# Optimization experiments

Measured on AMD Instinct MI355X. Metric: run time of the kernel, lower is better.

Reference implementation:

```python
import jax, jax.numpy as jnp
import numpy as np

D_MODEL = 4096
D_FF = 4 * D_MODEL
B, S = 2, 2048


def setup_inputs() -> dict:
    key = jax.random.key(0)
    kx, k1, kb1, k2, kb2 = jax.random.split(key, 5)
    s1 = 1.0 / np.sqrt(D_MODEL)
    s2 = 1.0 / np.sqrt(D_FF)
    return {
        "x": jax.random.normal(kx, (B, S, D_MODEL), dtype=jnp.float32),
        "W1": jax.random.normal(k1, (D_MODEL, D_FF), dtype=jnp.float32) * s1,
        "b1": jax.random.normal(kb1, (D_FF,), dtype=jnp.float32) * 0.01,
        "W2": jax.random.normal(k2, (D_FF, D_MODEL), dtype=jnp.float32) * s2,
        "b2": jax.random.normal(kb2, (D_MODEL,), dtype=jnp.float32) * 0.01,
    }


def reference(x, W1, b1, W2, b2):
    # FlashFFN: engine computes fc2(act(fc1(x) + b1)); host then nan-guards
    # and adds fc2_bias. GELU is the standard transformer FFN activation.
    orig_shape = x.shape
    flat_x = x.reshape(-1, D_MODEL)                      # [T, D]
    h = jax.nn.gelu(flat_x @ W1 + b1)                    # [T, 4D]
    y = h @ W2                                           # [T, D]
    y = jnp.nan_to_num(y, nan=0.0, posinf=0.0, neginf=0.0)
    return y.reshape(orig_shape) + b2
```

## Files before the change

### kernel.cpp

```cpp
#include <hip/hip_runtime.h>
#include <hip/hip_bf16.h>


using bf16 = __hip_bfloat16;
typedef __attribute__((ext_vector_type(4))) float floatx4;
typedef __attribute__((ext_vector_type(8))) short shortx8;

#define TOKENS 4096
#define DMODEL 4096
#define DFF    16384

__device__ __forceinline__ void gload_lds16(const void* g, void* l) {
  __builtin_amdgcn_global_load_lds(
      (const __attribute__((address_space(1))) unsigned int*)g,
      (__attribute__((address_space(3))) unsigned int*)l,
      16, 0, 0);
}

__device__ __forceinline__ unsigned lds_u32(const void* p) {
  return (unsigned)(unsigned long long)(const __attribute__((address_space(3))) char*)p;
}

__device__ __forceinline__ float gelu_tanh(float x) {
  float z = 0.7978845608028654f * (x + 0.044715f * x * x * x);
  float e = __expf(2.0f * z);
  float t = 1.0f - 2.0f / (e + 1.0f);
  return 0.5f * x * (1.0f + t);
}

#define DSR(dst, addr, off) \
  asm volatile("ds_read_b128 %0, %1 offset:" #off : "=v"(dst) : "v"(addr))

__global__ void cvt_f32_bf16(const float* __restrict__ in, bf16* __restrict__ out) {
  int i = (blockIdx.x * blockDim.x + threadIdx.x) * 8;
  float4 a = *(const float4*)(in + i);
  float4 b = *(const float4*)(in + i + 4);
  union { shortx8 v; bf16 h[8]; } r;
  r.h[0] = __float2bfloat16(a.x); r.h[1] = __float2bfloat16(a.y);
  r.h[2] = __float2bfloat16(a.z); r.h[3] = __float2bfloat16(a.w);
  r.h[4] = __float2bfloat16(b.x); r.h[5] = __float2bfloat16(b.y);
  r.h[6] = __float2bfloat16(b.z); r.h[7] = __float2bfloat16(b.w);
  *(shortx8*)(out + i) = r.v;
}

__global__ void transpose_cvt(const float* __restrict__ in, bf16* __restrict__ out,
                              int R, int C) {
  __shared__ float tile[64][65];
  const int c0 = blockIdx.x * 64, r0 = blockIdx.y * 64;
  const int t = threadIdx.x;
#pragma unroll
  for (int p = 0; p < 4; ++p) {
    int r = p * 16 + (t >> 4);
    int c = (t & 15) * 4;
    float4 v = *(const float4*)(in + (size_t)(r0 + r) * C + c0 + c);
    tile[r][c] = v.x; tile[r][c + 1] = v.y;
    tile[r][c + 2] = v.z; tile[r][c + 3] = v.w;
  }
  __syncthreads();
#pragma unroll
  for (int p = 0; p < 2; ++p) {
    int c = p * 32 + (t >> 3);
    int rb = (t & 7) * 8;
    union { shortx8 v; bf16 h[8]; } u;
#pragma unroll
    for (int j = 0; j < 8; ++j) u.h[j] = __float2bfloat16(tile[rb + j][c]);
    *(shortx8*)(out + (size_t)(c0 + c) * R + r0 + rb) = u.v;
  }
}

template <int FUSE_GELU>
__launch_bounds__(512, 2)
__global__ void gemm_bt(const bf16* __restrict__ A, const bf16* __restrict__ Bt,
                        const float* __restrict__ bias, void* __restrict__ Cout,
                        int M, int N, int K) {
  __shared__ __align__(16) bf16 As[2 * 2 * 128 * 64];
  __shared__ __align__(16) bf16 Bs[2 * 2 * 128 * 64];

  const int tid = threadIdx.x;
  const int wave = tid >> 6;
  const int lane = tid & 63;

  const int wg8  = blockIdx.x & 255;
  const int xcd  = wg8 & 7;
  const int slot = wg8 >> 3;
  const int m0 = (2 * xcd + (slot & 1)) * 256;
  const int n0 = ((blockIdx.x >> 8) * 16 + (slot >> 1)) * 256;

  const size_t Ks = (size_t)K;
  const int NT = K >> 6;

  const int swz = (lane & 7) ^ ((lane >> 3) & 7);
  const bf16* agp = A  + (size_t)(m0 + wave * 8 + (lane >> 3)) * Ks + swz * 8;
  const bf16* bgp = Bt + (size_t)(n0 + wave * 8 + (lane >> 3)) * Ks + swz * 8;

  const int wr = wave >> 2, wc = wave & 3;
  const int fr = lane & 15;
  const int q  = lane >> 4;
  const unsigned As0 = lds_u32(As);
  const unsigned Bs0 = lds_u32(Bs);
  const unsigned aK0 = As0 + (unsigned)((wr * 16 + fr) * 128 +
                       (((fr >> 2) & 1) * 64) + ((q ^ (fr & 3)) * 16));
  const unsigned aK1 = aK0 ^ 64u;
  const unsigned bK0 = Bs0 + (unsigned)((wc * 16 + fr) * 128 +
                       (((fr >> 2) & 1) * 64) + ((q ^ (fr & 3)) * 16));
  const unsigned bK1 = bK0 ^ 64u;

  floatx4 acc[8][4] = {};

  {
    bf16* lA = As + wave * 512;
    bf16* lB = Bs + wave * 512;
    gload_lds16(agp,             lA);
    gload_lds16(agp +  64 * Ks,  lA + 4096);
    gload_lds16(bgp,             lB);
    gload_lds16(bgp +  64 * Ks,  lB + 4096);
    gload_lds16(agp + 128 * Ks,  lA + 8192);
    gload_lds16(agp + 192 * Ks,  lA + 12288);
    gload_lds16(bgp + 128 * Ks,  lB + 8192);
    gload_lds16(bgp + 192 * Ks,  lB + 12288);
  }
  asm volatile("s_waitcnt vmcnt(4)");
  __builtin_amdgcn_s_barrier();

  for (int t = 0; t < NT; ++t) {
    const unsigned dsel = (unsigned)(t & 1) << 15;
    const unsigned a0 = aK0 + dsel, a1 = aK1 + dsel;
    const unsigned b0 = bK0 + dsel, b1 = bK1 + dsel;
    const bool st = (t + 1 < NT);
    const bf16* gA = agp + (size_t)(t + 1) * 64;
    const bf16* gB = bgp + (size_t)(t + 1) * 64;
    bf16* lA = As + ((t + 1) & 1) * 16384 + wave * 512;
    bf16* lB = Bs + ((t + 1) & 1) * 16384 + wave * 512;

    shortx8 A0[2][4], A1[2][4], B0[2][2], B1[2][2];

    DSR(A0[0][0], a0, 0);     DSR(A0[0][1], a0, 4096);
    DSR(A0[0][2], a0, 8192);  DSR(A0[0][3], a0, 12288);
    DSR(A0[1][0], a1, 0);     DSR(A0[1][1], a1, 4096);
    DSR(A0[1][2], a1, 8192);  DSR(A0[1][3], a1, 12288);
    DSR(B0[0][0], b0, 0);     DSR(B0[0][1], b0, 8192);
    DSR(B0[1][0], b1, 0);     DSR(B0[1][1], b1, 8192);
    if (st) { gload_lds16(gA, lA); gload_lds16(gA + 64 * Ks, lA + 4096); }
    __builtin_amdgcn_s_barrier();
    asm volatile("s_waitcnt lgkmcnt(0)");
    __builtin_amdgcn_sched_barrier(0);
    __builtin_amdgcn_s_setprio(1);
#pragma unroll
    for (int f = 0; f < 4; ++f)
#pragma unroll
      for (int n = 0; n < 2; ++n) {
        acc[f][n] = __builtin_amdgcn_mfma_f32_16x16x32_bf16(A0[0][f], B0[0][n], acc[f][n], 0, 0, 0);
        acc[f][n] = __builtin_amdgcn_mfma_f32_16x16x32_bf16(A0[1][f], B0[1][n], acc[f][n], 0, 0, 0);
      }
    __builtin_amdgcn_s_setprio(0);
    __builtin_amdgcn_sched_barrier(0);
    if (st) asm volatile("s_waitcnt vmcnt(4)");
    else    asm volatile("s_waitcnt vmcnt(2)");
    __builtin_amdgcn_s_barrier();

    DSR(A1[0][0], a0, 16384); DSR(A1[0][1], a0, 20480);
    DSR(A1[0][2], a0, 24576); DSR(A1[0][3], a0, 28672);
    DSR(A1[1][0], a1, 16384); DSR(A1[1][1], a1, 20480);
    DSR(A1[1][2], a1, 24576); DSR(A1[1][3], a1, 28672);
    if (st) { gload_lds16(gB, lB); gload_lds16(gB + 64 * Ks, lB + 4096); }
    __builtin_amdgcn_s_barrier();
    asm volatile("s_waitcnt lgkmcnt(0)");
    __builtin_amdgcn_sched_barrier(0);
    __builtin_amdgcn_s_setprio(1);
#pragma unroll
    for (int f = 0; f < 4; ++f)
#pragma unroll
      for (int n = 0; n < 2; ++n) {
        acc[4 + f][n] = __builtin_amdgcn_mfma_f32_16x16x32_bf16(A1[0][f], B0[0][n], acc[4 + f][n], 0, 0, 0);
        acc[4 + f][n] = __builtin_amdgcn_mfma_f32_16x16x32_bf16(A1[1][f], B0[1][n], acc[4 + f][n], 0, 0, 0);
      }
    __builtin_amdgcn_s_setprio(0);
    __builtin_amdgcn_sched_barrier(0);
    if (st) asm volatile("s_waitcnt vmcnt(4)");
    else    asm volatile("s_waitcnt vmcnt(0)");
    __builtin_amdgcn_s_barrier();

    DSR(B1[0][0], b0, 16384); DSR(B1[0][1], b0, 24576);
    DSR(B1[1][0], b1, 16384); DSR(B1[1][1], b1, 24576);
    if (st) { gload_lds16(gA + 128 * Ks, lA + 8192); gload_lds16(gA + 192 * Ks, lA + 12288); }
    __builtin_amdgcn_s_barrier();
    asm volatile("s_waitcnt lgkmcnt(0)");
    __builtin_amdgcn_sched_barrier(0);
    __builtin_amdgcn_s_setprio(1);
#pragma unroll
    for (int f = 0; f < 4; ++f)
#pragma unroll
      for (int n = 0; n < 2; ++n) {
        acc[f][2 + n] = __builtin_amdgcn_mfma_f32_16x16x32_bf16(A0[0][f], B1[0][n], acc[f][2 + n], 0, 0, 0);
        acc[f][2 + n] = __builtin_amdgcn_mfma_f32_16x16x32_bf16(A0[1][f], B1[1][n], acc[f][2 + n], 0, 0, 0);
      }
    __builtin_amdgcn_s_setprio(0);
    __builtin_amdgcn_sched_barrier(0);
    __builtin_amdgcn_s_barrier();

    if (st) { gload_lds16(gB + 128 * Ks, lB + 8192); gload_lds16(gB + 192 * Ks, lB + 12288); }
    __builtin_amdgcn_s_setprio(1);
#pragma unroll
    for (int f = 0; f < 4; ++f)
#pragma unroll
      for (int n = 0; n < 2; ++n) {
        acc[4 + f][2 + n] = __builtin_amdgcn_mfma_f32_16x16x32_bf16(A1[0][f], B1[0][n], acc[4 + f][2 + n], 0, 0, 0);
        acc[4 + f][2 + n] = __builtin_amdgcn_mfma_f32_16x16x32_bf16(A1[1][f], B1[1][n], acc[4 + f][2 + n], 0, 0, 0);
      }
    __builtin_amdgcn_s_setprio(0);
    __builtin_amdgcn_sched_barrier(0);
    if (st) asm volatile("s_waitcnt vmcnt(4)");
    __builtin_amdgcn_s_barrier();
  }

  const int col0 = n0 + wc * 16 + fr;
  const int row0 = m0 + wr * 16 + (lane >> 4) * 4;
#pragma unroll
  for (int ni = 0; ni < 4; ++ni) {
    const int col = col0 + ni * 64;
    const float bv = bias[col];
#pragma unroll
    for (int mi = 0; mi < 8; ++mi) {
#pragma unroll
      for (int r = 0; r < 4; ++r) {
        const int row = row0 + mi * 32 + r;
        float v = acc[mi][ni][r];
        if (FUSE_GELU) {
          v = gelu_tanh(v + bv);
          ((bf16*)Cout)[(size_t)row * N + col] = __float2bfloat16(v);
        } else {
          if (!isfinite(v)) v = 0.0f;
          ((float*)Cout)[(size_t)row * N + col] = v + bv;
        }
      }
    }
  }
}

extern "C" void kernel_launch(void* const* d_in, const int* in_sizes, int n_in,
                              void* d_out, int out_size, void* d_ws, size_t ws_size,
                              hipStream_t stream) {
  const float* x  = (const float*)d_in[0];
  const float* W1 = (const float*)d_in[1];
  const float* b1 = (const float*)d_in[2];
  const float* W2 = (const float*)d_in[3];
  const float* b2 = (const float*)d_in[4];
  float* out = (float*)d_out;

  char* ws = (char*)d_ws;
  bf16* xb  = (bf16*)(ws);
  bf16* h   = (bf16*)(ws + (size_t)32  * 1024 * 1024);
  bf16* w1t = (bf16*)(ws + (size_t)160 * 1024 * 1024);
  bf16* w2t = (bf16*)(ws + (size_t)288 * 1024 * 1024);

  cvt_f32_bf16<<<(TOKENS * DMODEL / 8) / 256, 256, 0, stream>>>(x, xb);
  transpose_cvt<<<dim3(DFF / 64, DMODEL / 64), 256, 0, stream>>>(W1, w1t, DMODEL, DFF);
  transpose_cvt<<<dim3(DMODEL / 64, DFF / 64), 256, 0, stream>>>(W2, w2t, DFF, DMODEL);

  gemm_bt<1><<<dim3((DFF / 256) * (TOKENS / 256)), 512, 0, stream>>>(
      xb, w1t, b1, h, TOKENS, DFF, DMODEL);

  gemm_bt<0><<<dim3((DMODEL / 256) * (TOKENS / 256)), 512, 0, stream>>>(
      h, w2t, b2, out, TOKENS, DMODEL, DFF);
}
```

Measured before the change: 1.103 ms.

## Software-pipeline LDS fragment reads to overlap with MFMA quadrants

Restructures the main GEMM loop so that LDS reads of the A0/B0 fragments for the next k-tile are issued during the current tile's later MFMA quadrants. Partial lgkmcnt waits replace full ones, and several barriers are dropped, so LDS latency is hidden behind matrix math rather than stalling it. It also reorders the global-to-LDS loads and changes the vmcnt thresholds. The cost is more live registers and trickier wait-count correctness: a miscounted vmcnt or lgkmcnt could read stale LDS data.

```diff
diff --git a/kernel.cpp b/kernel.cpp
--- a/kernel.cpp
+++ b/kernel.cpp
@@ -106,6 +106,7 @@
   const unsigned bK1 = bK0 ^ 64u;
 
   floatx4 acc[8][4] = {};
+  shortx8 A0[2][4], A1[2][4], B0[2][2], B1[2][2];
 
   {
     bf16* lA = As + wave * 512;
@@ -116,55 +117,60 @@
     gload_lds16(bgp +  64 * Ks,  lB + 4096);
     gload_lds16(agp + 128 * Ks,  lA + 8192);
     gload_lds16(agp + 192 * Ks,  lA + 12288);
+    gload_lds16(bgp,             lB);
+  }
+  {
+    bf16* lB = Bs + wave * 512;
     gload_lds16(bgp + 128 * Ks,  lB + 8192);
     gload_lds16(bgp + 192 * Ks,  lB + 12288);
   }
-  asm volatile("s_waitcnt vmcnt(4)");
+  asm volatile("s_waitcnt vmcnt(3)");
   __builtin_amdgcn_s_barrier();
+  DSR(B0[0][0], bK0, 0); DSR(B0[0][1], bK0, 8192);
+  DSR(B0[1][0], bK1, 0); DSR(B0[1][1], bK1, 8192);
+  DSR(A0[0][0], aK0, 0);     DSR(A0[0][1], aK0, 4096);
+  DSR(A0[0][2], aK0, 8192);  DSR(A0[0][3], aK0, 12288);
+  DSR(A0[1][0], aK1, 0);     DSR(A0[1][1], aK1, 4096);
+  DSR(A0[1][2], aK1, 8192);  DSR(A0[1][3], aK1, 12288);
 
   for (int t = 0; t < NT; ++t) {
-    const unsigned dsel = (unsigned)(t & 1) << 15;
-    const unsigned a0 = aK0 + dsel, a1 = aK1 + dsel;
-    const unsigned b0 = bK0 + dsel, b1 = bK1 + dsel;
+    const unsigned dsel  = (unsigned)(t & 1) << 15;
+    const unsigned dseln = (unsigned)((t + 1) & 1) << 15;
+    const unsigned a0 = aK0 + dsel,  a1 = aK1 + dsel;
+    const unsigned b0 = bK0 + dsel,  b1 = bK1 + dsel;
+    const unsigned an0 = aK0 + dseln, an1 = aK1 + dseln;
+    const unsigned bn0 = bK0 + dseln, bn1 = bK1 + dseln;
     const bool st = (t + 1 < NT);
     const bf16* gA = agp + (size_t)(t + 1) * 64;
     const bf16* gB = bgp + (size_t)(t + 1) * 64;
     bf16* lA = As + ((t + 1) & 1) * 16384 + wave * 512;
     bf16* lB = Bs + ((t + 1) & 1) * 16384 + wave * 512;
 
-    shortx8 A0[2][4], A1[2][4], B0[2][2], B1[2][2];
-
-    DSR(A0[0][0], a0, 0);     DSR(A0[0][1], a0, 4096);
-    DSR(A0[0][2], a0, 8192);  DSR(A0[0][3], a0, 12288);
-    DSR(A0[1][0], a1, 0);     DSR(A0[1][1], a1, 4096);
-    DSR(A0[1][2], a1, 8192);  DSR(A0[1][3], a1, 12288);
-    DSR(B0[0][0], b0, 0);     DSR(B0[0][1], b0, 8192);
-    DSR(B0[1][0], b1, 0);     DSR(B0[1][1], b1, 8192);
-    if (st) { gload_lds16(gA, lA); gload_lds16(gA + 64 * Ks, lA + 4096); }
-    __builtin_amdgcn_s_barrier();
-    asm volatile("s_waitcnt lgkmcnt(0)");
-    __builtin_amdgcn_sched_barrier(0);
-    __builtin_amdgcn_s_setprio(1);
-#pragma unroll
-    for (int f = 0; f < 4; ++f)
-#pragma unroll
-      for (int n = 0; n < 2; ++n) {
-        acc[f][n] = __builtin_amdgcn_mfma_f32_16x16x32_bf16(A0[0][f], B0[0][n], acc[f][n], 0, 0, 0);
-        acc[f][n] = __builtin_amdgcn_mfma_f32_16x16x32_bf16(A0[1][f], B0[1][n], acc[f][n], 0, 0, 0);
-      }
-    __builtin_amdgcn_s_setprio(0);
-    __builtin_amdgcn_sched_barrier(0);
-    if (st) asm volatile("s_waitcnt vmcnt(4)");
-    else    asm volatile("s_waitcnt vmcnt(2)");
-    __builtin_amdgcn_s_barrier();
-
     DSR(A1[0][0], a0, 16384); DSR(A1[0][1], a0, 20480);
     DSR(A1[0][2], a0, 24576); DSR(A1[0][3], a0, 28672);
     DSR(A1[1][0], a1, 16384); DSR(A1[1][1], a1, 20480);
     DSR(A1[1][2], a1, 24576); DSR(A1[1][3], a1, 28672);
     if (st) { gload_lds16(gB, lB); gload_lds16(gB + 64 * Ks, lB + 4096); }
-    __builtin_amdgcn_s_barrier();
-    asm volatile("s_waitcnt lgkmcnt(0)");
+    asm volatile("s_waitcnt lgkmcnt(8)");
+    __builtin_amdgcn_sched_barrier(0);
+    __builtin_amdgcn_s_setprio(1);
+#pragma unroll
+    for (int f = 0; f < 4; ++f)
+#pragma unroll
+      for (int n = 0; n < 2; ++n) {
+        acc[f][n] = __builtin_amdgcn_mfma_f32_16x16x32_bf16(A0[0][f], B0[0][n], acc[f][n], 0, 0, 0);
+        acc[f][n] = __builtin_amdgcn_mfma_f32_16x16x32_bf16(A0[1][f], B0[1][n], acc[f][n], 0, 0, 0);
+      }
+    __builtin_amdgcn_s_setprio(0);
+    __builtin_amdgcn_sched_barrier(0);
+    if (st) asm volatile("s_waitcnt vmcnt(2)");
+    else    asm volatile("s_waitcnt vmcnt(0)");
+    __builtin_amdgcn_s_barrier();
+
+    DSR(B1[0][0], b0, 16384); DSR(B1[0][1], b0, 24576);
+    DSR(B1[1][0], b1, 16384); DSR(B1[1][1], b1, 24576);
+    if (st) { gload_lds16(gA, lA); gload_lds16(gA + 64 * Ks, lA + 4096); }
+    asm volatile("s_waitcnt lgkmcnt(4)");
     __builtin_amdgcn_sched_barrier(0);
     __builtin_amdgcn_s_setprio(1);
 #pragma unroll
@@ -176,16 +182,33 @@
       }
     __builtin_amdgcn_s_setprio(0);
     __builtin_amdgcn_sched_barrier(0);
-    if (st) asm volatile("s_waitcnt vmcnt(4)");
-    else    asm volatile("s_waitcnt vmcnt(0)");
-    __builtin_amdgcn_s_barrier();
-
-    DSR(B1[0][0], b0, 16384); DSR(B1[0][1], b0, 24576);
-    DSR(B1[1][0], b1, 16384); DSR(B1[1][1], b1, 24576);
-    if (st) { gload_lds16(gA + 128 * Ks, lA + 8192); gload_lds16(gA + 192 * Ks, lA + 12288); }
-    __builtin_amdgcn_s_barrier();
-    asm volatile("s_waitcnt lgkmcnt(0)");
-    __builtin_amdgcn_sched_barrier(0);
+    if (st) asm volatile("s_waitcnt vmcnt(2)");
+    __builtin_amdgcn_s_barrier();
+
+    if (st) {
+      DSR(B0[0][0], bn0, 0); DSR(B0[0][1], bn0, 8192);
+      DSR(B0[1][0], bn1, 0); DSR(B0[1][1], bn1, 8192);
+      gload_lds16(gA + 128 * Ks, lA + 8192);
+      gload_lds16(gA + 192 * Ks, lA + 12288);
+      asm volatile("s_waitcnt lgkmcnt(4)");
+    } else {
+      asm volatile("s_waitcnt lgkmcnt(0)");
+    }
+    __builtin_amdgcn_sched_barrier(0);
+    __builtin_amdgcn_s_setprio(1);
+#pragma unroll
+    for (int f = 0; f < 4; ++f)
+#pragma unroll
+      for (int n = 0; n < 2; ++n) {
+        acc[4 + f][2 + n] = __builtin_amdgcn_mfma_f32_16x16x32_bf16(A1[0][f], B1[0][n], acc[4 + f][2 + n], 0, 0, 0);
+        acc[4 + f][2 + n] = __builtin_amdgcn_mfma_f32_16x16x32_bf16(A1[1][f], B1[1][n], acc[4 + f][2 + n], 0, 0, 0);
+      }
+    __builtin_amdgcn_s_setprio(0);
+    __builtin_amdgcn_sched_barrier(0);
+    if (st) asm volatile("s_waitcnt vmcnt(2)");
+    __builtin_amdgcn_s_barrier();
+
+    if (st) { gload_lds16(gB + 128 * Ks, lB + 8192); gload_lds16(gB + 192 * Ks, lB + 12288); }
     __builtin_amdgcn_s_setprio(1);
 #pragma unroll
     for (int f = 0; f < 4; ++f)
@@ -196,20 +219,13 @@
       }
     __builtin_amdgcn_s_setprio(0);
     __builtin_amdgcn_sched_barrier(0);
-    __builtin_amdgcn_s_barrier();
-
-    if (st) { gload_lds16(gB + 128 * Ks, lB + 8192); gload_lds16(gB + 192 * Ks, lB + 12288); }
-    __builtin_amdgcn_s_setprio(1);
-#pragma unroll
-    for (int f = 0; f < 4; ++f)
-#pragma unroll
-      for (int n = 0; n < 2; ++n) {
-        acc[4 + f][2 + n] = __builtin_amdgcn_mfma_f32_16x16x32_bf16(A1[0][f], B1[0][n], acc[4 + f][2 + n], 0, 0, 0);
-        acc[4 + f][2 + n] = __builtin_amdgcn_mfma_f32_16x16x32_bf16(A1[1][f], B1[1][n], acc[4 + f][2 + n], 0, 0, 0);
-      }
-    __builtin_amdgcn_s_setprio(0);
-    __builtin_amdgcn_sched_barrier(0);
-    if (st) asm volatile("s_waitcnt vmcnt(4)");
+    if (st) {
+      DSR(A0[0][0], an0, 0);     DSR(A0[0][1], an0, 4096);
+      DSR(A0[0][2], an0, 8192);  DSR(A0[0][3], an0, 12288);
+      DSR(A0[1][0], an1, 0);     DSR(A0[1][1], an1, 4096);
+      DSR(A0[1][2], an1, 8192);  DSR(A0[1][3], an1, 12288);
+      asm volatile("s_waitcnt vmcnt(2)");
+    }
     __builtin_amdgcn_s_barrier();
   }
 
```

New measurement: 1.097 ms. Within noise of the previous version (-0.5%).

## Software-pipeline LDS fragment reads across K-tiles and unroll by two

Applied to the files above, without the earlier changes.

Restructures the GEMM main loop so LDS fragment reads for the next K-tile are issued during the current tile's MFMA phases, with partial lgkmcnt waits instead of full drains. Barriers per tile drop from seven to four, and B loads for tile t+2 are prefetched early. The loop is unrolled by two with compile-time LDS offsets so buffer selection needs no runtime add. This adds register pressure from fragments live across iterations and assumes NT is even. The waitcnt and barrier ordering is delicate and could race if a count is off.

```diff
diff --git a/kernel.cpp b/kernel.cpp
--- a/kernel.cpp
+++ b/kernel.cpp
@@ -28,8 +28,8 @@
   return 0.5f * x * (1.0f + t);
 }
 
-#define DSR(dst, addr, off) \
-  asm volatile("ds_read_b128 %0, %1 offset:" #off : "=v"(dst) : "v"(addr))
+#define DSRI(dst, addr, off) \
+  asm volatile("ds_read_b128 %0, %1 offset:%c2" : "=v"(dst) : "v"(addr), "i"(off))
 
 __global__ void cvt_f32_bf16(const float* __restrict__ in, bf16* __restrict__ out) {
   int i = (blockIdx.x * blockDim.x + threadIdx.x) * 8;
@@ -67,6 +67,114 @@
     *(shortx8*)(out + (size_t)(c0 + c) * R + r0 + rb) = u.v;
   }
 }
+
+#define TILE_BODY(T, D, DN)                                                     \
+  {                                                                             \
+    const int t_ = (T);                                                         \
+    const bool st  = (t_ + 1 < NT);                                             \
+    const bool st2 = (t_ + 2 < NT);                                             \
+    const bf16* gA = agp + (size_t)(t_ + 1) * 64;                               \
+    bf16* lA = As + (DN / 2) + wave * 512;                                      \
+    bf16* lB = Bs + (DN / 2) + wave * 512;                                      \
+              \
+    DSRI(A1[0][0], aK0, (D) + 16384); DSRI(A1[0][1], aK0, (D) + 20480);         \
+    DSRI(A1[0][2], aK0, (D) + 24576); DSRI(A1[0][3], aK0, (D) + 28672);         \
+    DSRI(A1[1][0], aK1, (D) + 16384); DSRI(A1[1][1], aK1, (D) + 20480);         \
+    DSRI(A1[1][2], aK1, (D) + 24576); DSRI(A1[1][3], aK1, (D) + 28672);         \
+    if (st) { gload_lds16(gA, lA); gload_lds16(gA + 64 * Ks, lA + 4096); }      \
+    asm volatile("s_waitcnt lgkmcnt(8)");      \
+    __builtin_amdgcn_sched_barrier(0);                      \
+    __builtin_amdgcn_s_setprio(1);                                              \
+    _Pragma("unroll")                                                           \
+    for (int f = 0; f < 4; ++f)                                                 \
+      _Pragma("unroll")                                                         \
+      for (int n = 0; n < 2; ++n)                                               \
+        acc[f][n] = __builtin_amdgcn_mfma_f32_16x16x32_bf16(A0[0][f], B0[0][n], acc[f][n], 0, 0, 0); \
+    _Pragma("unroll")                                                           \
+    for (int f = 0; f < 4; ++f)                                                 \
+      _Pragma("unroll")                                                         \
+      for (int n = 0; n < 2; ++n)                                               \
+        acc[f][n] = __builtin_amdgcn_mfma_f32_16x16x32_bf16(A0[1][f], B0[1][n], acc[f][n], 0, 0, 0); \
+    __builtin_amdgcn_s_setprio(0);                                              \
+    if (st) asm volatile("s_waitcnt vmcnt(4)");            \
+    else    asm volatile("s_waitcnt vmcnt(0)");                                 \
+    __builtin_amdgcn_s_barrier();                                               \
+              \
+    DSRI(B1[0][0], bK0, (D) + 16384); DSRI(B1[0][1], bK0, (D) + 24576);         \
+    DSRI(B1[1][0], bK1, (D) + 16384); DSRI(B1[1][1], bK1, (D) + 24576);         \
+    if (st) { gload_lds16(gA + 128 * Ks, lA + 8192);                            \
+              gload_lds16(gA + 192 * Ks, lA + 12288); }                         \
+    asm volatile("s_waitcnt lgkmcnt(4)");            \
+    __builtin_amdgcn_sched_barrier(0);                                          \
+    __builtin_amdgcn_s_setprio(1);                                              \
+    _Pragma("unroll")                                                           \
+    for (int f = 0; f < 4; ++f)                                                 \
+      _Pragma("unroll")                                                         \
+      for (int n = 0; n < 2; ++n)                                               \
+        acc[4 + f][n] = __builtin_amdgcn_mfma_f32_16x16x32_bf16(A1[0][f], B0[0][n], acc[4 + f][n], 0, 0, 0); \
+    _Pragma("unroll")                                                           \
+    for (int f = 0; f < 4; ++f)                                                 \
+      _Pragma("unroll")                                                         \
+      for (int n = 0; n < 2; ++n)                                               \
+        acc[4 + f][n] = __builtin_amdgcn_mfma_f32_16x16x32_bf16(A1[1][f], B0[1][n], acc[4 + f][n], 0, 0, 0); \
+    __builtin_amdgcn_s_setprio(0);                                              \
+    if (st) asm volatile("s_waitcnt vmcnt(4)");          \
+    __builtin_amdgcn_s_barrier();                                               \
+            \
+    if (st) {                                                                   \
+      const bf16* gB = bgp + (size_t)(t_ + 1) * 64;                             \
+      DSRI(B0[0][0], bK0, (DN) + 0); DSRI(B0[0][1], bK0, (DN) + 8192);          \
+      DSRI(B0[1][0], bK1, (DN) + 0); DSRI(B0[1][1], bK1, (DN) + 8192);          \
+      gload_lds16(gB + 128 * Ks, lB + 8192);                                    \
+      gload_lds16(gB + 192 * Ks, lB + 12288);                                   \
+      asm volatile("s_waitcnt lgkmcnt(4)");         \
+    } else {                                                                    \
+      asm volatile("s_waitcnt lgkmcnt(0)");                                     \
+    }                                                                           \
+    __builtin_amdgcn_sched_barrier(0);                                          \
+    __builtin_amdgcn_s_setprio(1);                                              \
+    _Pragma("unroll")                                                           \
+    for (int f = 0; f < 4; ++f)                                                 \
+      _Pragma("unroll")                                                         \
+      for (int n = 0; n < 2; ++n)                                               \
+        acc[4 + f][2 + n] = __builtin_amdgcn_mfma_f32_16x16x32_bf16(A1[0][f], B1[0][n], acc[4 + f][2 + n], 0, 0, 0); \
+    _Pragma("unroll")                                                           \
+    for (int f = 0; f < 4; ++f)                                                 \
+      _Pragma("unroll")                                                         \
+      for (int n = 0; n < 2; ++n)                                               \
+        acc[4 + f][2 + n] = __builtin_amdgcn_mfma_f32_16x16x32_bf16(A1[1][f], B1[1][n], acc[4 + f][2 + n], 0, 0, 0); \
+    __builtin_amdgcn_s_setprio(0);                                              \
+    if (st) asm volatile("s_waitcnt vmcnt(4)");          \
+    __builtin_amdgcn_s_barrier();                                               \
+           \
+    if (st2) {                                                                  \
+      const bf16* gB2 = bgp + (size_t)(t_ + 2) * 64;                            \
+      bf16* lB2 = Bs + ((D) / 2) + wave * 512;              \
+      gload_lds16(gB2,           lB2);                                          \
+      gload_lds16(gB2 + 64 * Ks, lB2 + 4096);                                   \
+    }                                                                           \
+    __builtin_amdgcn_s_setprio(1);                                              \
+    _Pragma("unroll")                                                           \
+    for (int f = 0; f < 4; ++f)                                                 \
+      _Pragma("unroll")                                                         \
+      for (int n = 0; n < 2; ++n)                                               \
+        acc[f][2 + n] = __builtin_amdgcn_mfma_f32_16x16x32_bf16(A0[0][f], B1[0][n], acc[f][2 + n], 0, 0, 0); \
+    _Pragma("unroll")                                                           \
+    for (int f = 0; f < 4; ++f)                                                 \
+      _Pragma("unroll")                                                         \
+      for (int n = 0; n < 2; ++n)                                               \
+        acc[f][2 + n] = __builtin_amdgcn_mfma_f32_16x16x32_bf16(A0[1][f], B1[1][n], acc[f][2 + n], 0, 0, 0); \
+    __builtin_amdgcn_s_setprio(0);                                              \
+    if (st) {                \
+      DSRI(A0[0][0], aK0, (DN) + 0);    DSRI(A0[0][1], aK0, (DN) + 4096);       \
+      DSRI(A0[0][2], aK0, (DN) + 8192); DSRI(A0[0][3], aK0, (DN) + 12288);      \
+      DSRI(A0[1][0], aK1, (DN) + 0);    DSRI(A0[1][1], aK1, (DN) + 4096);       \
+      DSRI(A0[1][2], aK1, (DN) + 8192); DSRI(A0[1][3], aK1, (DN) + 12288);      \
+    }                                                                           \
+    if (st2)     asm volatile("s_waitcnt vmcnt(4)");     \
+    else if (st) asm volatile("s_waitcnt vmcnt(2)");                            \
+    __builtin_amdgcn_s_barrier();                                               \
+  }
 
 template <int FUSE_GELU>
 __launch_bounds__(512, 2)
@@ -106,6 +214,7 @@
   const unsigned bK1 = bK0 ^ 64u;
 
   floatx4 acc[8][4] = {};
+  shortx8 A0[2][4], A1[2][4], B0[2][2], B1[2][2];
 
   {
     bf16* lA = As + wave * 512;
@@ -118,99 +227,26 @@
     gload_lds16(agp + 192 * Ks,  lA + 12288);
     gload_lds16(bgp + 128 * Ks,  lB + 8192);
     gload_lds16(bgp + 192 * Ks,  lB + 12288);
-  }
-  asm volatile("s_waitcnt vmcnt(4)");
+    if (NT > 1) {
+      bf16* lB1 = Bs + 16384 + wave * 512;
+      const bf16* gB1 = bgp + 64;
+      gload_lds16(gB1,           lB1);
+      gload_lds16(gB1 + 64 * Ks, lB1 + 4096);
+    }
+  }
+  if (NT > 1) asm volatile("s_waitcnt vmcnt(4)");
+  else        asm volatile("s_waitcnt vmcnt(2)");
   __builtin_amdgcn_s_barrier();
-
-  for (int t = 0; t < NT; ++t) {
-    const unsigned dsel = (unsigned)(t & 1) << 15;
-    const unsigned a0 = aK0 + dsel, a1 = aK1 + dsel;
-    const unsigned b0 = bK0 + dsel, b1 = bK1 + dsel;
-    const bool st = (t + 1 < NT);
-    const bf16* gA = agp + (size_t)(t + 1) * 64;
-    const bf16* gB = bgp + (size_t)(t + 1) * 64;
-    bf16* lA = As + ((t + 1) & 1) * 16384 + wave * 512;
-    bf16* lB = Bs + ((t + 1) & 1) * 16384 + wave * 512;
-
-    shortx8 A0[2][4], A1[2][4], B0[2][2], B1[2][2];
-
-    DSR(A0[0][0], a0, 0);     DSR(A0[0][1], a0, 4096);
-    DSR(A0[0][2], a0, 8192);  DSR(A0[0][3], a0, 12288);
-    DSR(A0[1][0], a1, 0);     DSR(A0[1][1], a1, 4096);
-    DSR(A0[1][2], a1, 8192);  DSR(A0[1][3], a1, 12288);
-    DSR(B0[0][0], b0, 0);     DSR(B0[0][1], b0, 8192);
-    DSR(B0[1][0], b1, 0);     DSR(B0[1][1], b1, 8192);
-    if (st) { gload_lds16(gA, lA); gload_lds16(gA + 64 * Ks, lA + 4096); }
-    __builtin_amdgcn_s_barrier();
-    asm volatile("s_waitcnt lgkmcnt(0)");
-    __builtin_amdgcn_sched_barrier(0);
-    __builtin_amdgcn_s_setprio(1);
-#pragma unroll
-    for (int f = 0; f < 4; ++f)
-#pragma unroll
-      for (int n = 0; n < 2; ++n) {
-        acc[f][n] = __builtin_amdgcn_mfma_f32_16x16x32_bf16(A0[0][f], B0[0][n], acc[f][n], 0, 0, 0);
-        acc[f][n] = __builtin_amdgcn_mfma_f32_16x16x32_bf16(A0[1][f], B0[1][n], acc[f][n], 0, 0, 0);
-      }
-    __builtin_amdgcn_s_setprio(0);
-    __builtin_amdgcn_sched_barrier(0);
-    if (st) asm volatile("s_waitcnt vmcnt(4)");
-    else    asm volatile("s_waitcnt vmcnt(2)");
-    __builtin_amdgcn_s_barrier();
-
-    DSR(A1[0][0], a0, 16384); DSR(A1[0][1], a0, 20480);
-    DSR(A1[0][2], a0, 24576); DSR(A1[0][3], a0, 28672);
-    DSR(A1[1][0], a1, 16384); DSR(A1[1][1], a1, 20480);
-    DSR(A1[1][2], a1, 24576); DSR(A1[1][3], a1, 28672);
-    if (st) { gload_lds16(gB, lB); gload_lds16(gB + 64 * Ks, lB + 4096); }
-    __builtin_amdgcn_s_barrier();
-    asm volatile("s_waitcnt lgkmcnt(0)");
-    __builtin_amdgcn_sched_barrier(0);
-    __builtin_amdgcn_s_setprio(1);
-#pragma unroll
-    for (int f = 0; f < 4; ++f)
-#pragma unroll
-      for (int n = 0; n < 2; ++n) {
-        acc[4 + f][n] = __builtin_amdgcn_mfma_f32_16x16x32_bf16(A1[0][f], B0[0][n], acc[4 + f][n], 0, 0, 0);
-        acc[4 + f][n] = __builtin_amdgcn_mfma_f32_16x16x32_bf16(A1[1][f], B0[1][n], acc[4 + f][n], 0, 0, 0);
-      }
-    __builtin_amdgcn_s_setprio(0);
-    __builtin_amdgcn_sched_barrier(0);
-    if (st) asm volatile("s_waitcnt vmcnt(4)");
-    else    asm volatile("s_waitcnt vmcnt(0)");
-    __builtin_amdgcn_s_barrier();
-
-    DSR(B1[0][0], b0, 16384); DSR(B1[0][1], b0, 24576);
-    DSR(B1[1][0], b1, 16384); DSR(B1[1][1], b1, 24576);
-    if (st) { gload_lds16(gA + 128 * Ks, lA + 8192); gload_lds16(gA + 192 * Ks, lA + 12288); }
-    __builtin_amdgcn_s_barrier();
-    asm volatile("s_waitcnt lgkmcnt(0)");
-    __builtin_amdgcn_sched_barrier(0);
-    __builtin_amdgcn_s_setprio(1);
-#pragma unroll
-    for (int f = 0; f < 4; ++f)
-#pragma unroll
-      for (int n = 0; n < 2; ++n) {
-        acc[f][2 + n] = __builtin_amdgcn_mfma_f32_16x16x32_bf16(A0[0][f], B1[0][n], acc[f][2 + n], 0, 0, 0);
-        acc[f][2 + n] = __builtin_amdgcn_mfma_f32_16x16x32_bf16(A0[1][f], B1[1][n], acc[f][2 + n], 0, 0, 0);
-      }
-    __builtin_amdgcn_s_setprio(0);
-    __builtin_amdgcn_sched_barrier(0);
-    __builtin_amdgcn_s_barrier();
-
-    if (st) { gload_lds16(gB + 128 * Ks, lB + 8192); gload_lds16(gB + 192 * Ks, lB + 12288); }
-    __builtin_amdgcn_s_setprio(1);
-#pragma unroll
-    for (int f = 0; f < 4; ++f)
-#pragma unroll
-      for (int n = 0; n < 2; ++n) {
-        acc[4 + f][2 + n] = __builtin_amdgcn_mfma_f32_16x16x32_bf16(A1[0][f], B1[0][n], acc[4 + f][2 + n], 0, 0, 0);
-        acc[4 + f][2 + n] = __builtin_amdgcn_mfma_f32_16x16x32_bf16(A1[1][f], B1[1][n], acc[4 + f][2 + n], 0, 0, 0);
-      }
-    __builtin_amdgcn_s_setprio(0);
-    __builtin_amdgcn_sched_barrier(0);
-    if (st) asm volatile("s_waitcnt vmcnt(4)");
-    __builtin_amdgcn_s_barrier();
+  DSRI(B0[0][0], bK0, 0); DSRI(B0[0][1], bK0, 8192);
+  DSRI(B0[1][0], bK1, 0); DSRI(B0[1][1], bK1, 8192);
+  DSRI(A0[0][0], aK0, 0);    DSRI(A0[0][1], aK0, 4096);
+  DSRI(A0[0][2], aK0, 8192); DSRI(A0[0][3], aK0, 12288);
+  DSRI(A0[1][0], aK1, 0);    DSRI(A0[1][1], aK1, 4096);
+  DSRI(A0[1][2], aK1, 8192); DSRI(A0[1][3], aK1, 12288);
+
+  for (int t = 0; t < NT; t += 2) {
+    TILE_BODY(t,     0,     32768)
+    TILE_BODY(t + 1, 32768, 0)
   }
 
   const int col0 = n0 + wc * 16 + fr;
```

Measured after the change: 2.682 ms. +143.2%, slower.
